# Optimization experiments

Hardware: AMD Instinct MI355X
Metric: run time of the kernel (lower is better)

Reference implementation:

```python
import jax, jax.numpy as jnp
import numpy as np

B, T = 128, 50
VOCAB, EMB_D, GRU_H = 10000, 200, 100
HEADS, AHID, THID = 8, 96, 96

def _conv(x, w, b, pad):
    y = jax.lax.conv_general_dilated(x, w, (1, 1), pad,
        dimension_numbers=('NCHW', 'OIHW', 'NCHW'))
    return y + b[None, :, None, None]

def _bn(x, g, b, m, v):
    s = jax.lax.rsqrt(v + 1e-5)
    return (x - m[None, :, None, None]) * (g * s)[None, :, None, None] + b[None, :, None, None]

def _maxpool(x):
    return jax.lax.reduce_window(x, -jnp.inf, jax.lax.max, (1, 1, 2, 2), (1, 1, 2, 2), 'VALID')

def _resize(x):
    # F.interpolate(mode='bilinear', align_corners=False) == half-pixel bilinear, no antialias
    return jax.image.resize(x, (x.shape[0], x.shape[1], 25, 156), 'bilinear', antialias=False)

def _audio_attn(x, wq, bq, wk, bk, wv, bv):
    # x: [B,96,H,W]; wq: [heads,96,96] == stacked per-head 1x1 convs
    Q = jnp.einsum('bchw,noc->bnohw', x, wq) + bq[None, :, :, None, None]
    K = jnp.einsum('bchw,noc->bnohw', x, wk) + bk[None, :, :, None, None]
    V = jnp.einsum('bchw,noc->bnohw', x, wv) + bv[None, :, :, None, None]
    # torch F.softmax with no dim on a 4D tensor defaults to dim=1 (channels) -> axis=2 here
    return jax.nn.softmax(Q * K, axis=2) * V  # [B,heads,96,H,W]

def _text_attn(o, wq, bq, wk, bk, wv, bv):
    # o: [N,100]; wq: [heads,96,100] == stacked per-head Linear layers
    Q = jnp.einsum('nd,hod->nho', o, wq) + bq[None]
    K = jnp.einsum('nd,hod->nho', o, wk) + bk[None]
    V = jnp.einsum('nd,hod->nho', o, wv) + bv[None]
    a = jax.nn.softmax(Q * K, axis=2) * V  # 2D softmax default dim=1 -> over feature axis
    return a.reshape(o.shape[0], -1)  # head-concat order == torch cat along dim=1

def _gru(xs, w_ih, w_hh, b_ih, b_hh):
    # xs: [T,B,200]; torch gate order r, z, n; b_hn applied inside r-gating
    def step(h, x):
        gi = x @ w_ih.T + b_ih
        gh = h @ w_hh.T + b_hh
        ir, iz, inew = jnp.split(gi, 3, axis=1)
        hr, hz, hnew = jnp.split(gh, 3, axis=1)
        r = jax.nn.sigmoid(ir + hr)
        z = jax.nn.sigmoid(iz + hz)
        n = jnp.tanh(inew + r * hnew)
        h2 = (1.0 - z) * n + z * h
        return h2, h2
    h0 = jnp.zeros((xs.shape[1], GRU_H), xs.dtype)
    hT, outs = jax.lax.scan(step, h0, xs)
    return outs, hT

def _forward(tokens, lengths, mfcc_t, mfcc_f, mfcc_c, w1a, b1a, g1a, be1a, m1a, v1a, w1b, b1b, g1b, be1b, m1b, v1b, w2, b2, g2, be2, m2, v2, w3, b3, g3, be3, m3, v3, w4, b4, g4, be4, m4, v4, wq_a1, bq_a1, wk_a1, bk_a1, wv_a1, bv_a1, wq_a2, bq_a2, wk_a2, bk_a2, wv_a2, bv_a2, emb, w_ih, w_hh, b_ih, b_hh, wq_t1, bq_t1, wk_t1, bk_t1, wv_t1, bv_t1, wq_t2, bq_t2, wk_t2, bk_t2, wv_t2, bv_t2, w_fa, b_fa, w_ft, b_ft, w_e, b_e):
    # --- audio CNN stem (eval-mode batchnorm; dropout off) ---
    xa = jax.nn.relu(_bn(_conv(mfcc_t, w1a, b1a, 'VALID'), g1a, be1a, m1a, v1a))
    xb = jax.nn.relu(_bn(_conv(mfcc_f, w1b, b1b, 'VALID'), g1b, be1b, m1b, v1b))
    # NOTE: original source reuses conv1b/bn1b for the third input (faithful to that)
    xc = jax.nn.relu(_bn(_conv(mfcc_c, w1b, b1b, 'VALID'), g1b, be1b, m1b, v1b))
    x = jnp.concatenate([_resize(xa), _resize(xb), _resize(xc)], axis=1)  # [B,24,25,156]
    x = _maxpool(jax.nn.relu(_bn(_conv(x, w2, b2, [(1, 1), (1, 1)]), g2, be2, m2, v2)))  # [B,32,12,78]
    x = _maxpool(jax.nn.relu(_bn(_conv(x, w3, b3, [(1, 1), (1, 1)]), g3, be3, m3, v3)))  # [B,64,6,39]
    x = jax.nn.relu(_bn(_conv(x, w4, b4, [(1, 1), (1, 1)]), g4, be4, m4, v4))            # [B,96,6,39]
    # --- two stacked per-head audio attentions, then per-head spatial GAP ---
    a1 = _audio_attn(x, wq_a1, bq_a1, wk_a1, bk_a1, wv_a1, bv_a1).mean(axis=(-2, -1))  # [B,8,96]
    a2 = _audio_attn(x, wq_a2, bq_a2, wk_a2, bk_a2, wv_a2, bv_a2).mean(axis=(-2, -1))
    # forward() slices heads along the height concat and GAPs -> per head [stage1 96, stage2 96]
    self_attn_audio = jnp.concatenate([a1, a2], axis=2).reshape(x.shape[0], -1)  # [B,1536]
    # --- text branch: embedding + GRU (all lengths == T -> pack/pad is identity) ---
    ex = jnp.swapaxes(emb[tokens], 0, 1)  # [T,B,200]
    outs, h = _gru(ex, w_ih, w_hh, b_ih, b_hh)  # h: [B,100]
    output = jnp.swapaxes(outs, 0, 1).reshape(-1, GRU_H)  # [B*T,100]
    t1 = _text_attn(output, wq_t1, bq_t1, wk_t1, bk_t1, wv_t1, bv_t1)
    t2 = _text_attn(output, wq_t2, bq_t2, wk_t2, bk_t2, wv_t2, bv_t2)
    self_attn_text = jnp.concatenate([t1, t2], axis=1).reshape(x.shape[0], T, -1).sum(axis=1)  # [B,1536]
    # --- cross-modal gated fusion ---
    x_gap = x.mean(axis=(-2, -1))  # [B,96]
    a_text = jax.nn.softmax(x_gap @ w_fa.T + b_fa, axis=1)   # [B,100]
    attn_text_based_audio = a_text * h                        # [B,100]
    a_audio = jax.nn.softmax(h @ w_ft.T + b_ft, axis=1)      # [B,96]
    attn_audio_based_text = a_audio * x_gap                   # [B,96]
    feat = jnp.concatenate([self_attn_audio, self_attn_text,
                            attn_audio_based_text, attn_text_based_audio], axis=1)  # [B,3268]
    return feat @ w_e.T + b_e  # [B,4] emotion logits

def setup_inputs() -> dict:
    key = jax.random.key(0)
    ks = iter(jax.random.split(key, 100))
    nrm = lambda s, sc=0.05: jax.random.normal(next(ks), s, jnp.float32) * sc
    uni = lambda s: jax.random.uniform(next(ks), s, jnp.float32) * 0.5 + 0.5
    d = {}
    d['mfcc_t'] = jax.random.normal(next(ks), (B, 1, 200, 40), jnp.float32)
    d['mfcc_f'] = jax.random.normal(next(ks), (B, 1, 200, 40), jnp.float32)
    d['mfcc_c'] = jax.random.normal(next(ks), (B, 1, 200, 40), jnp.float32)
    d['tokens'] = jax.random.randint(next(ks), (B, T), 0, VOCAB)
    d['lengths'] = jnp.full((B,), T, jnp.int32)
    def bnp(pre, c):
        d['g' + pre] = 1.0 + nrm((c,)); d['be' + pre] = nrm((c,))
        d['m' + pre] = nrm((c,)); d['v' + pre] = uni((c,))
    d['w1a'] = nrm((8, 1, 5, 2), 0.2); d['b1a'] = nrm((8,)); bnp('1a', 8)
    d['w1b'] = nrm((8, 1, 2, 6), 0.2); d['b1b'] = nrm((8,)); bnp('1b', 8)
    d['w2'] = nrm((32, 24, 3, 3), 0.1); d['b2'] = nrm((32,)); bnp('2', 32)
    d['w3'] = nrm((64, 32, 3, 3), 0.1); d['b3'] = nrm((64,)); bnp('3', 64)
    d['w4'] = nrm((96, 64, 3, 3), 0.08); d['b4'] = nrm((96,)); bnp('4', 96)
    for s in ('1', '2'):
        for p in ('q', 'k', 'v'):
            d['w%s_a%s' % (p, s)] = nrm((HEADS, 96, 96), 0.1)
            d['b%s_a%s' % (p, s)] = nrm((HEADS, 96))
    d['emb'] = nrm((VOCAB, EMB_D), 0.1)
    d['w_ih'] = nrm((3 * GRU_H, EMB_D), 0.1); d['w_hh'] = nrm((3 * GRU_H, GRU_H), 0.1)
    d['b_ih'] = nrm((3 * GRU_H,)); d['b_hh'] = nrm((3 * GRU_H,))
    for s in ('1', '2'):
        for p in ('q', 'k', 'v'):
            d['w%s_t%s' % (p, s)] = nrm((HEADS, THID, GRU_H), 0.1)
            d['b%s_t%s' % (p, s)] = nrm((HEADS, THID))
    d['w_fa'] = nrm((100, 96), 0.1); d['b_fa'] = nrm((100,))
    d['w_ft'] = nrm((96, 100), 0.1); d['b_ft'] = nrm((96,))
    d['w_e'] = nrm((4, 2 * HEADS * AHID + 2 * HEADS * THID + 96 + 100), 0.05); d['b_e'] = nrm((4,))
    return d

def reference(mfcc_t, mfcc_f, mfcc_c, tokens, lengths, w1a, b1a, g1a, be1a, m1a, v1a, w1b, b1b, g1b, be1b, m1b, v1b, w2, b2, g2, be2, m2, v2, w3, b3, g3, be3, m3, v3, w4, b4, g4, be4, m4, v4, wq_a1, bq_a1, wk_a1, bk_a1, wv_a1, bv_a1, wq_a2, bq_a2, wk_a2, bk_a2, wv_a2, bv_a2, emb, w_ih, w_hh, b_ih, b_hh, wq_t1, bq_t1, wk_t1, bk_t1, wv_t1, bv_t1, wq_t2, bq_t2, wk_t2, bk_t2, wv_t2, bv_t2, w_fa, b_fa, w_ft, b_ft, w_e, b_e):
    return _forward(tokens, lengths, mfcc_t, mfcc_f, mfcc_c, w1a, b1a, g1a, be1a, m1a, v1a, w1b, b1b, g1b, be1b, m1b, v1b, w2, b2, g2, be2, m2, v2, w3, b3, g3, be3, m3, v3, w4, b4, g4, be4, m4, v4, wq_a1, bq_a1, wk_a1, bk_a1, wv_a1, bv_a1, wq_a2, bq_a2, wk_a2, bk_a2, wv_a2, bv_a2, emb, w_ih, w_hh, b_ih, b_hh, wq_t1, bq_t1, wk_t1, bk_t1, wv_t1, bv_t1, wq_t2, bq_t2, wk_t2, bk_t2, wv_t2, bv_t2, w_fa, b_fa, w_ft, b_ft, w_e, b_e)
```

## Files before the change

kernel.cpp:

```cpp
#include <hip/hip_runtime.h>
#include <math.h>

static constexpr int kB = 128;
static constexpr int kT = 50;

struct TDesc { const float* src; float* dst; int O; int C; int total; };
struct TPack { TDesc d[15]; };
__global__ void k_transpose_pack(TPack p) {
    TDesc t = p.d[blockIdx.y];
    int idx = blockIdx.x * 256 + threadIdx.x;
    if (idx >= t.total) return;
    int o = idx % t.O; int r = idx / t.O; int c = r % t.C; int n = r / t.C;
    t.dst[idx] = t.src[((size_t)n * t.O + o) * t.C + c];
}

__global__ void k_stem(const float* __restrict__ mt, const float* __restrict__ mf,
                       const float* __restrict__ mc,
                       const float* __restrict__ w1a, const float* __restrict__ b1a,
                       const float* __restrict__ g1a, const float* __restrict__ be1a,
                       const float* __restrict__ m1a, const float* __restrict__ v1a,
                       const float* __restrict__ w1b, const float* __restrict__ b1b,
                       const float* __restrict__ g1b, const float* __restrict__ be1b,
                       const float* __restrict__ m1b, const float* __restrict__ v1b,
                       float* __restrict__ out, int total) {
    int idx = blockIdx.x * blockDim.x + threadIdx.x;
    if (idx >= total) return;
    int ox = idx % 156; int t = idx / 156;
    int oy = t % 25; t /= 25;
    int ch = t % 24; int b = t / 24;
    int grp = ch >> 3, c = ch & 7;
    const float* src; int Hc, Wc;
    const float *wb, *cb, *g, *be, *m, *v;
    if (grp == 0) { src = mt; Hc = 196; Wc = 39; wb = w1a + c * 10;
                    cb = b1a; g = g1a; be = be1a; m = m1a; v = v1a; }
    else          { src = (grp == 1 ? mf : mc); Hc = 199; Wc = 35; wb = w1b + c * 12;
                    cb = b1b; g = g1b; be = be1b; m = m1b; v = v1b; }
    float s = g[c] * rsqrtf(v[c] + 1e-5f);
    float bias = (cb[c] - m[c]) * s + be[c];
    float sy = (oy + 0.5f) * ((float)Hc / 25.f) - 0.5f;
    float sx = (ox + 0.5f) * ((float)Wc / 156.f) - 0.5f;
    float fy0 = floorf(sy), fx0 = floorf(sx);
    float fy = sy - fy0, fx = sx - fx0;
    int y0 = (int)fy0, x0 = (int)fx0;
    int y0c = min(max(y0, 0), Hc - 1), y1c = min(max(y0 + 1, 0), Hc - 1);
    int x0c = min(max(x0, 0), Wc - 1), x1c = min(max(x0 + 1, 0), Wc - 1);
    bool xs = (x1c == x0c), ys = (y1c == y0c);
    const float* p = src + (size_t)b * 8000;
    float t00, t01, t10, t11;
    if (grp == 0) {
        float W[6][3];
        #pragma unroll
        for (int r = 0; r < 6; ++r) {
            int rr = min(y0c + r, 199);
            #pragma unroll
            for (int cc = 0; cc < 3; ++cc)
                W[r][cc] = p[rr * 40 + min(x0c + cc, 39)];
        }
        float a00 = 0.f, a01 = 0.f, a10 = 0.f, a11 = 0.f;
        #pragma unroll
        for (int ky = 0; ky < 5; ++ky)
            #pragma unroll
            for (int kx = 0; kx < 2; ++kx) {
                float wv = wb[ky * 2 + kx];
                a00 += W[ky][kx] * wv;     a01 += W[ky][kx + 1] * wv;
                a10 += W[ky + 1][kx] * wv; a11 += W[ky + 1][kx + 1] * wv;
            }
        t00 = a00;
        t01 = xs ? a00 : a01;
        t10 = ys ? a00 : a10;
        t11 = xs ? (ys ? a00 : a10) : (ys ? a01 : a11);
    } else {
        float W[3][7];
        #pragma unroll
        for (int r = 0; r < 3; ++r) {
            int rr = min(y0c + r, 199);
            #pragma unroll
            for (int cc = 0; cc < 7; ++cc)
                W[r][cc] = p[rr * 40 + min(x0c + cc, 39)];
        }
        float a00 = 0.f, a01 = 0.f, a10 = 0.f, a11 = 0.f;
        #pragma unroll
        for (int ky = 0; ky < 2; ++ky)
            #pragma unroll
            for (int kx = 0; kx < 6; ++kx) {
                float wv = wb[ky * 6 + kx];
                a00 += W[ky][kx] * wv;     a01 += W[ky][kx + 1] * wv;
                a10 += W[ky + 1][kx] * wv; a11 += W[ky + 1][kx + 1] * wv;
            }
        t00 = a00;
        t01 = xs ? a00 : a01;
        t10 = ys ? a00 : a10;
        t11 = xs ? (ys ? a00 : a10) : (ys ? a01 : a11);
    }
    float r00 = fmaxf(t00 * s + bias, 0.f), r01 = fmaxf(t01 * s + bias, 0.f);
    float r10 = fmaxf(t10 * s + bias, 0.f), r11 = fmaxf(t11 * s + bias, 0.f);
    out[idx] = r00 * (1.f - fy) * (1.f - fx) + r01 * (1.f - fy) * fx
// ... 20 lines not shown
    for (int j = 0; j < NPX; ++j) {
        int px = tid + j * 256;
        int oy = px / W, ox = px - oy * W;
        bool ok = (px < ROWS * W) && (row0 + oy < H);
        val[j] = ok;
        off[j] = ok ? (oy * WP + ox) : 0;
    }

    float acc[NPX][8];
    #pragma unroll
    for (int j = 0; j < NPX; ++j)
        #pragma unroll
        for (int o = 0; o < 8; ++o) acc[j][o] = 0.f;

    for (int c0 = 0; c0 < CIN; c0 += CI_T) {
        __syncthreads();
        for (int e = tid; e < STAGE; e += 256) {
            int ci = e / (RP * WP);
            int rem = e - ci * RP * WP;
            int r = rem / WP;
            int xx = rem - r * WP;
            int iy = row0 - 1 + r;
            int ix = xx - 1;
            float vv = 0.f;
            if (iy >= 0 && iy < H && ix >= 0 && ix < W)
                vv = in[((size_t)(b * CIN + c0 + ci) * H + iy) * W + ix];
            sx[e] = vv;
        }
        for (int e = tid; e < CI_T * 9 * 8; e += 256) {
            int rk = e >> 3;
            int o = e & 7;
            sw[e] = wT[((size_t)c0 * 9 + rk) * COUT + oc0 + o];
        }
        __syncthreads();
        #pragma unroll 1
        for (int cl = 0; cl < CI_T; ++cl) {
            const float* sxc = sx + cl * RP * WP;
            #pragma unroll
            for (int k = 0; k < 9; ++k) {
                const int ky = k / 3, kx = k % 3;
                const float4 wa = *(const float4*)(sw + (cl * 9 + k) * 8);
                const float4 wb = *(const float4*)(sw + (cl * 9 + k) * 8 + 4);
                #pragma unroll
                for (int j = 0; j < NPX; ++j) {
                    float xv = sxc[off[j] + ky * WP + kx];
                    acc[j][0] += xv * wa.x; acc[j][1] += xv * wa.y;
                    acc[j][2] += xv * wa.z; acc[j][3] += xv * wa.w;
                    acc[j][4] += xv * wb.x; acc[j][5] += xv * wb.y;
                    acc[j][6] += xv * wb.z; acc[j][7] += xv * wb.w;
                }
            }
        }
    }
    float sc[8], bi[8];
    #pragma unroll
    for (int o = 0; o < 8; ++o) {
        float s = g[oc0 + o] * rsqrtf(v[oc0 + o] + 1e-5f);
        sc[o] = s; bi[o] = (cb[oc0 + o] - m[oc0 + o]) * s + be[oc0 + o];
    }
    #pragma unroll
    for (int j = 0; j < NPX; ++j) if (val[j]) {
        int px = tid + j * 256;
        int oy = row0 + px / W, ox = px % W;
        #pragma unroll
        for (int o = 0; o < 8; ++o)
            out[((size_t)(b * COUT + oc0 + o) * H + oy) * W + ox] =
                fmaxf(acc[j][o] * sc[o] + bi[o], 0.f);
    }
}

__global__ void k_maxpool(const float* __restrict__ in, float* __restrict__ out,
                          int C, int Hin, int Win, int Hout, int Wout, int total) {
    int idx = blockIdx.x * blockDim.x + threadIdx.x;
    if (idx >= total) return;
    int ox = idx % Wout; int t = idx / Wout;
    int oy = t % Hout; t /= Hout;
    int c = t % C; int b = t / C;
    const float* p = in + ((size_t)(b * C + c) * Hin + 2 * oy) * Win + 2 * ox;
    float m0 = fmaxf(p[0], p[1]);
    float m1 = fmaxf(p[Win], p[Win + 1]);
    out[idx] = fmaxf(m0, m1);
}

__global__ void __launch_bounds__(128) k_audio_attn(
    const float* __restrict__ x,
    const float* __restrict__ wq1, const float* __restrict__ bq1,
    const float* __restrict__ wk1, const float* __restrict__ bk1,
    const float* __restrict__ wv1, const float* __restrict__ bv1,
    const float* __restrict__ wq2, const float* __restrict__ bq2,
    const float* __restrict__ wk2, const float* __restrict__ bk2,
    const float* __restrict__ wv2, const float* __restrict__ bv2,
    float* __restrict__ afeat, float* __restrict__ xgap) {
    int b = blockIdx.x, n = blockIdx.y, stage = blockIdx.z;
    const float* wq = stage ? wq2 : wq1; const float* bq = stage ? bq2 : bq1;
    const float* wk = stage ? wk2 : wk1; const float* bk = stage ? bk2 : bk1;
    const float* wv = stage ? wv2 : wv1; const float* bv = stage ? bv2 : bv1;
    __shared__ float xt[96 * 28];
    __shared__ float sb[96 * 27];
    __shared__ float pmax[4][26], psum[4][26];
    __shared__ float mx[26], sm[26];
    int tid = threadIdx.x;
    bool act = tid < 96;
    int o = act ? tid : 0;
    float bqv = act ? bq[n * 96 + tid] : 0.f;
    float bkv = act ? bk[n * 96 + tid] : 0.f;
    float bvv = act ? bv[n * 96 + tid] : 0.f;
    const float* wqb = wq + n * 9216 + o;
    const float* wkb = wk + n * 9216 + o;
    const float* wvb = wv + n * 9216 + o;
    const bool do_gap = (n == 0 && stage == 0);
    float accO = 0.f, xsum = 0.f;
    const float* xb = x + (size_t)b * 96 * 234;
    for (int tile = 0; tile < 9; ++tile) {
        int p0 = tile * 26;
        __syncthreads();
        for (int e = tid; e < 2496; e += 128) {
            int c = e / 26, pp = e - c * 26;
            xt[c * 28 + pp] = xb[c * 234 + p0 + pp];
        }
        __syncthreads();
        if (do_gap && act) {
            const float* xr = xt + o * 28;
            #pragma unroll
            for (int p = 0; p < 26; ++p) xsum += xr[p];
        }
        float aq[26], ak[26], av[26];
        #pragma unroll
        for (int p = 0; p < 26; ++p) { aq[p] = bqv; ak[p] = bkv; av[p] = bvv; }
        for (int c = 0; c < 96; ++c) {
            float wqv = wqb[c * 96], wkv = wkb[c * 96], wvv2 = wvb[c * 96];
            const float* xr = xt + c * 28;
            #pragma unroll
            for (int q4 = 0; q4 < 6; ++q4) {
                float4 x4 = *(const float4*)(xr + q4 * 4);
                int p = q4 * 4;
                aq[p]   += wqv * x4.x; ak[p]   += wkv * x4.x; av[p]   += wvv2 * x4.x;
                aq[p+1] += wqv * x4.y; ak[p+1] += wkv * x4.y; av[p+1] += wvv2 * x4.y;
                aq[p+2] += wqv * x4.z; ak[p+2] += wkv * x4.z; av[p+2] += wvv2 * x4.z;
                aq[p+3] += wqv * x4.w; ak[p+3] += wkv * x4.w; av[p+3] += wvv2 * x4.w;
            }
            float2 x2 = *(const float2*)(xr + 24);
            aq[24] += wqv * x2.x; ak[24] += wkv * x2.x; av[24] += wvv2 * x2.x;
            aq[25] += wqv * x2.y; ak[25] += wkv * x2.y; av[25] += wvv2 * x2.y;
        }
        if (act) {
            #pragma unroll
            for (int p = 0; p < 26; ++p)
                sb[o * 27 + p] = aq[p] * ak[p];
        }
        __syncthreads();
        if (tid < 104) {
            int p = tid % 26, ch = tid / 26;
            int o0 = ch * 24;
            float m_ = -1e30f;
            for (int q = 0; q < 24; ++q) m_ = fmaxf(m_, sb[(o0 + q) * 27 + p]);
            pmax[ch][p] = m_;
        }
        __syncthreads();
        if (tid < 26)
            mx[tid] = fmaxf(fmaxf(pmax[0][tid], pmax[1][tid]),
                            fmaxf(pmax[2][tid], pmax[3][tid]));
        __syncthreads();
        if (tid < 104) {
            int p = tid % 26, ch = tid / 26;
            int o0 = ch * 24;
            float mv = mx[p];
            float s_ = 0.f;
            for (int q = 0; q < 24; ++q) s_ += __expf(sb[(o0 + q) * 27 + p] - mv);
            psum[ch][p] = s_;
        }
        __syncthreads();
        if (tid < 26)
            sm[tid] = psum[0][tid] + psum[1][tid] + psum[2][tid] + psum[3][tid];
        __syncthreads();
        if (act) {
            #pragma unroll
            for (int p = 0; p < 26; ++p)
                accO += __expf(sb[o * 27 + p] - mx[p]) / sm[p] * av[p];
        }
    }
    if (act) afeat[b * 1536 + n * 192 + stage * 96 + tid] = accO * (1.f / 234.f);
    if (do_gap && act) xgap[b * 96 + tid] = xsum * (1.f / 234.f);
}

__global__ void __launch_bounds__(320) k_gi(const int* __restrict__ tokens,
        const float* __restrict__ emb, const float* __restrict__ w_ih,
        const float* __restrict__ b_ih, float* __restrict__ GI) {
    int r0 = blockIdx.x * 8;
    int tid = threadIdx.x;
    __shared__ float er[8][200];
    for (int e = tid; e < 1600; e += 320) {
        int r = e / 200, c = e - r * 200;
        er[r][c] = emb[(size_t)tokens[r0 + r] * 200 + c];
    }
    __syncthreads();
    if (tid < 300) {
        float acc[8];
        float bv = b_ih[tid];
        #pragma unroll
        for (int r = 0; r < 8; ++r) acc[r] = bv;
        for (int k4 = 0; k4 < 50; ++k4) {
            float4 w4 = *(const float4*)(w_ih + (size_t)tid * 200 + k4 * 4);
            #pragma unroll
            for (int r = 0; r < 8; ++r) {
                float4 x4 = *(const float4*)&er[r][k4 * 4];
                acc[r] += w4.x * x4.x + w4.y * x4.y + w4.z * x4.z + w4.w * x4.w;
            }
        }
        #pragma unroll
        for (int r = 0; r < 8; ++r)
            GI[(size_t)(r0 + r) * 300 + tid] = acc[r];
    }
}

__global__ void __launch_bounds__(320) k_gru_all(const float* __restrict__ GI,
        const float* __restrict__ w_hh, const float* __restrict__ b_hh,
        float* __restrict__ outs) {
    int b = blockIdx.x, tid = threadIdx.x;
    __shared__ float hs[100];
    __shared__ float gH[300];
    float4 wreg[25];
    float bias = 0.f;
    if (tid < 300) {
        bias = b_hh[tid];
        #pragma unroll
        for (int k4 = 0; k4 < 25; ++k4)
            wreg[k4] = *(const float4*)(w_hh + (size_t)tid * 100 + k4 * 4);
    }
    if (tid < 100) hs[tid] = 0.f;
    __syncthreads();
    for (int t = 0; t < kT; ++t) {
        if (tid < 300) {
            float gh = bias;
            #pragma unroll
            for (int k4 = 0; k4 < 25; ++k4) {
                float4 h4 = *(const float4*)&hs[k4 * 4];
                gh += wreg[k4].x * h4.x + wreg[k4].y * h4.y
                    + wreg[k4].z * h4.z + wreg[k4].w * h4.w;
            }
            gH[tid] = gh;
        }
        __syncthreads();
        if (tid < 100) {
            const float* gi = GI + ((size_t)b * kT + t) * 300;
            float r = 1.f / (1.f + expf(-(gi[tid] + gH[tid])));
            float z = 1.f / (1.f + expf(-(gi[100 + tid] + gH[100 + tid])));
            float nn = tanhf(gi[200 + tid] + r * gH[200 + tid]);
            float h2 = (1.f - z) * nn + z * hs[tid];
            hs[tid] = h2;
            outs[((size_t)b * kT + t) * 100 + tid] = h2;
        }
        __syncthreads();
    }
}

__global__ void __launch_bounds__(128) k_text_attn(const float* __restrict__ outs,
    const float* __restrict__ wq1, const float* __restrict__ bq1,
    const float* __restrict__ wk1, const float* __restrict__ bk1,
    const float* __restrict__ wv1, const float* __restrict__ bv1,
    const float* __restrict__ wq2, const float* __restrict__ bq2,
    const float* __restrict__ wk2, const float* __restrict__ bk2,
    const float* __restrict__ wv2, const float* __restrict__ bv2,
    float* __restrict__ tfeat) {
    int b = blockIdx.x, stage = blockIdx.y, n = blockIdx.z;
    const float* wq = stage ? wq2 : wq1; const float* bq = stage ? bq2 : bq1;
// ... 107 lines not shown
    }
    __syncthreads();
    if (tid < 100) atba[tid] = expf(st[tid] - redm[0]) / reds[0] * hv[tid];
    if (tid < 96)  aat[tid]  = expf(sa[tid] - redm[1]) / reds[1] * xg[tid];
    __syncthreads();
    float a0 = 0.f, a1 = 0.f, a2 = 0.f, a3 = 0.f;
    for (int col = tid; col < 3268; col += 128) {
        float f;
        if (col < 1536)      f = afeat[b * 1536 + col];
        else if (col < 3072) f = tfeat[b * 1536 + col - 1536];
        else if (col < 3168) f = aat[col - 3072];
        else                 f = atba[col - 3168];
        a0 += w_e[col] * f;            a1 += w_e[3268 + col] * f;
        a2 += w_e[2 * 3268 + col] * f; a3 += w_e[3 * 3268 + col] * f;
    }
    __shared__ float r4[4][128];
    r4[0][tid] = a0; r4[1][tid] = a1; r4[2][tid] = a2; r4[3][tid] = a3;
    __syncthreads();
    if (tid < 4) {
        float s = 0.f;
        for (int i = 0; i < 128; ++i) s += r4[tid][i];
        out[b * 4 + tid] = s + b_e[tid];
    }
}

extern "C" void kernel_launch(void* const* d_in, const int* in_sizes, int n_in,
                              void* d_out, int out_size, void* d_ws, size_t ws_size,
                              hipStream_t stream) {
    (void)in_sizes; (void)n_in; (void)out_size; (void)ws_size;
    const float* mfcc_t = (const float*)d_in[0];
    const float* mfcc_f = (const float*)d_in[1];
    const float* mfcc_c = (const float*)d_in[2];
    const int*   tokens = (const int*)d_in[3];
    const float *w1a = (const float*)d_in[5],  *b1a = (const float*)d_in[6],
                *g1a = (const float*)d_in[7],  *be1a = (const float*)d_in[8],
                *m1a = (const float*)d_in[9],  *v1a = (const float*)d_in[10];
    const float *w1b = (const float*)d_in[11], *b1b = (const float*)d_in[12],
                *g1b = (const float*)d_in[13], *be1b = (const float*)d_in[14],
                *m1b = (const float*)d_in[15], *v1b = (const float*)d_in[16];
    const float *w2 = (const float*)d_in[17], *b2 = (const float*)d_in[18],
                *g2 = (const float*)d_in[19], *be2 = (const float*)d_in[20],
                *m2 = (const float*)d_in[21], *v2 = (const float*)d_in[22];
    const float *w3 = (const float*)d_in[23], *b3 = (const float*)d_in[24],
                *g3 = (const float*)d_in[25], *be3 = (const float*)d_in[26],
                *m3 = (const float*)d_in[27], *v3 = (const float*)d_in[28];
    const float *w4 = (const float*)d_in[29], *b4 = (const float*)d_in[30],
                *g4 = (const float*)d_in[31], *be4 = (const float*)d_in[32],
                *m4 = (const float*)d_in[33], *v4 = (const float*)d_in[34];
    const float *wq_a1 = (const float*)d_in[35], *bq_a1 = (const float*)d_in[36],
                *wk_a1 = (const float*)d_in[37], *bk_a1 = (const float*)d_in[38],
                *wv_a1 = (const float*)d_in[39], *bv_a1 = (const float*)d_in[40];
    const float *wq_a2 = (const float*)d_in[41], *bq_a2 = (const float*)d_in[42],
                *wk_a2 = (const float*)d_in[43], *bk_a2 = (const float*)d_in[44],
                *wv_a2 = (const float*)d_in[45], *bv_a2 = (const float*)d_in[46];
    const float *emb  = (const float*)d_in[47];
    const float *w_ih = (const float*)d_in[48], *w_hh = (const float*)d_in[49],
                *b_ih = (const float*)d_in[50], *b_hh = (const float*)d_in[51];
    const float *wq_t1 = (const float*)d_in[52], *bq_t1 = (const float*)d_in[53],
                *wk_t1 = (const float*)d_in[54], *bk_t1 = (const float*)d_in[55],
                *wv_t1 = (const float*)d_in[56], *bv_t1 = (const float*)d_in[57];
    const float *wq_t2 = (const float*)d_in[58], *bq_t2 = (const float*)d_in[59],
                *wk_t2 = (const float*)d_in[60], *bk_t2 = (const float*)d_in[61],
                *wv_t2 = (const float*)d_in[62], *bv_t2 = (const float*)d_in[63];
    const float *w_fa = (const float*)d_in[64], *b_fa = (const float*)d_in[65],
                *w_ft = (const float*)d_in[66], *b_ft = (const float*)d_in[67],
                *w_e  = (const float*)d_in[68], *b_e  = (const float*)d_in[69];

    float* ws = (float*)d_ws;
    const size_t Z0 = 0;
    const size_t Z1 = 22091776ull;
    const size_t OUTS  = 34072576ull;
    const size_t AFEAT = 34712576ull;
    const size_t TFEAT = 34909184ull;
    const size_t XGAP  = 35105792ull;
    const size_t WT    = 35118080ull;
    float* X1 = ws + Z1;
    float* C2 = ws + Z0;  float* P2 = ws + Z1;
    float* C3 = ws + Z0;  float* P3 = ws + Z1;
    float* X4 = ws + Z0;  float* GI = ws + Z1;
    float* outs  = ws + OUTS;
    float* afeat = ws + AFEAT;
    float* tfeat = ws + TFEAT;
    float* xgap  = ws + XGAP;
    float* wqa1t = ws + WT;
    float* wka1t = wqa1t + 73728; float* wva1t = wka1t + 73728;
    float* wqa2t = wva1t + 73728; float* wka2t = wqa2t + 73728; float* wva2t = wka2t + 73728;
    float* wqt1t = wva2t + 73728;
    float* wkt1t = wqt1t + 76800; float* wvt1t = wkt1t + 76800;
    float* wqt2t = wvt1t + 76800; float* wkt2t = wqt2t + 76800; float* wvt2t = wkt2t + 76800;
    float* wT2 = outs;
    float* wT3 = outs + 6912;
    float* wT4 = outs + 25344;

    TPack tp;
    tp.d[0]  = {wq_a1, wqa1t, 96, 96, 73728};
    tp.d[1]  = {wk_a1, wka1t, 96, 96, 73728};
    tp.d[2]  = {wv_a1, wva1t, 96, 96, 73728};
    tp.d[3]  = {wq_a2, wqa2t, 96, 96, 73728};
    tp.d[4]  = {wk_a2, wka2t, 96, 96, 73728};
    tp.d[5]  = {wv_a2, wva2t, 96, 96, 73728};
    tp.d[6]  = {w2, wT2, 32, 216, 6912};
    tp.d[7]  = {w3, wT3, 64, 288, 18432};
    tp.d[8]  = {w4, wT4, 96, 576, 55296};
    tp.d[9]  = {wq_t1, wqt1t, 96, 100, 76800};
    tp.d[10] = {wk_t1, wkt1t, 96, 100, 76800};
    tp.d[11] = {wv_t1, wvt1t, 96, 100, 76800};
    tp.d[12] = {wq_t2, wqt2t, 96, 100, 76800};
    tp.d[13] = {wk_t2, wkt2t, 96, 100, 76800};
    tp.d[14] = {wv_t2, wvt2t, 96, 100, 76800};
    k_transpose_pack<<<dim3(300, 15), 256, 0, stream>>>(tp);

    k_stem<<<46800, 256, 0, stream>>>(mfcc_t, mfcc_f, mfcc_c,
        w1a, b1a, g1a, be1a, m1a, v1a,
        w1b, b1b, g1b, be1b, m1b, v1b, X1, 11980800);
    k_conv3x3_tiled<24, 8, 25, 156, 9, 6><<<dim3(128, 3, 4), 256, 0, stream>>>(
        X1, wT2, b2, g2, be2, m2, v2, C2, 32);
    k_maxpool<<<14976, 256, 0, stream>>>(C2, P2, 32, 25, 156, 12, 78, 3833856);
    k_conv3x3_tiled<32, 8, 12, 78, 12, 4><<<dim3(128, 1, 8), 256, 0, stream>>>(
        P2, wT3, b3, g3, be3, m3, v3, C3, 64);
    k_maxpool<<<7488, 256, 0, stream>>>(C3, P3, 64, 12, 78, 6, 39, 1916928);
    k_conv3x3_tiled<64, 16, 6, 39, 6, 1><<<dim3(128, 1, 12), 256, 0, stream>>>(
        P3, wT4, b4, g4, be4, m4, v4, X4, 96);

    k_audio_attn<<<dim3(kB, 8, 2), 128, 0, stream>>>(X4,
        wqa1t, bq_a1, wka1t, bk_a1, wva1t, bv_a1,
        wqa2t, bq_a2, wka2t, bk_a2, wva2t, bv_a2, afeat, xgap);

    k_gi<<<kB * kT / 8, 320, 0, stream>>>(tokens, emb, w_ih, b_ih, GI);
    k_gru_all<<<kB, 320, 0, stream>>>(GI, w_hh, b_hh, outs);
    k_text_attn<<<dim3(kB, 2, 8), 128, 0, stream>>>(outs,
        wqt1t, bq_t1, wkt1t, bk_t1, wvt1t, bv_t1,
        wqt2t, bq_t2, wkt2t, bk_t2, wvt2t, bv_t2, tfeat);

    k_final<<<kB, 128, 0, stream>>>(xgap, outs, afeat, tfeat,
                                    w_fa, b_fa, w_ft, b_ft, w_e, b_e, (float*)d_out);
}
```

Before: 1.571 ms.

## Restructure audio attention kernel to parallelize over positions with atomic reductions

The audio attention kernel now splits each batch item's 234 spatial positions across 4 blocks of 256 threads. Each thread holds one position's 96 channels in registers and reads untransposed weight rows staged through shared memory with a register prefetch. The softmax over channels is computed in a single pass, and the per-channel mean over positions is reduced with wave shuffles plus atomicAdd into a buffer zeroed beforehand. This exposes more parallelism and drops the per-tile syncs and the audio weight transposes, in exchange for a large register footprint, atomics, and an extra zeroing launch.

```diff
diff --git a/kernel.cpp b/kernel.cpp
--- a/kernel.cpp
+++ b/kernel.cpp
@@ -5,13 +5,19 @@
 static constexpr int kT = 50;
 
 struct TDesc { const float* src; float* dst; int O; int C; int total; };
-struct TPack { TDesc d[15]; };
+struct TPack { TDesc d[9]; };
 __global__ void k_transpose_pack(TPack p) {
     TDesc t = p.d[blockIdx.y];
     int idx = blockIdx.x * 256 + threadIdx.x;
     if (idx >= t.total) return;
     int o = idx % t.O; int r = idx / t.O; int c = r % t.C; int n = r / t.C;
     t.dst[idx] = t.src[((size_t)n * t.O + o) * t.C + c];
+}
+
+__global__ void k_zero2(float* __restrict__ a, int na, float* __restrict__ b, int nb) {
+    int i = blockIdx.x * 256 + threadIdx.x;
+    if (i < na) a[i] = 0.f;
+    if (i < nb) b[i] = 0.f;
 }
 
 __global__ void k_stem(const float* __restrict__ mt, const float* __restrict__ mf,
@@ -198,7 +204,7 @@
     out[idx] = fmaxf(m0, m1);
 }
 
-__global__ void __launch_bounds__(128) k_audio_attn(
+__global__ void __launch_bounds__(256, 2) k_audio_attn(
     const float* __restrict__ x,
     const float* __restrict__ wq1, const float* __restrict__ bq1,
     const float* __restrict__ wk1, const float* __restrict__ bk1,
@@ -207,96 +213,165 @@
     const float* __restrict__ wk2, const float* __restrict__ bk2,
     const float* __restrict__ wv2, const float* __restrict__ bv2,
     float* __restrict__ afeat, float* __restrict__ xgap) {
-    int b = blockIdx.x, n = blockIdx.y, stage = blockIdx.z;
+    const int b = blockIdx.x >> 2, pt = blockIdx.x & 3;
+    const int n = blockIdx.y, stage = blockIdx.z;
     const float* wq = stage ? wq2 : wq1; const float* bq = stage ? bq2 : bq1;
     const float* wk = stage ? wk2 : wk1; const float* bk = stage ? bk2 : bk1;
     const float* wv = stage ? wv2 : wv1; const float* bv = stage ? bv2 : bv1;
-    __shared__ float xt[96 * 28];
-    __shared__ float sb[96 * 27];
-    __shared__ float pmax[4][26], psum[4][26];
-    __shared__ float mx[26], sm[26];
-    int tid = threadIdx.x;
-    bool act = tid < 96;
-    int o = act ? tid : 0;
-    float bqv = act ? bq[n * 96 + tid] : 0.f;
-    float bkv = act ? bk[n * 96 + tid] : 0.f;
-    float bvv = act ? bv[n * 96 + tid] : 0.f;
-    const float* wqb = wq + n * 9216 + o;
-    const float* wkb = wk + n * 9216 + o;
-    const float* wvb = wv + n * 9216 + o;
-    const bool do_gap = (n == 0 && stage == 0);
-    float accO = 0.f, xsum = 0.f;
-    const float* xb = x + (size_t)b * 96 * 234;
-    for (int tile = 0; tile < 9; ++tile) {
-        int p0 = tile * 26;
-        __syncthreads();
-        for (int e = tid; e < 2496; e += 128) {
-            int c = e / 26, pp = e - c * 26;
-            xt[c * 28 + pp] = xb[c * 234 + p0 + pp];
-        }
-        __syncthreads();
-        if (do_gap && act) {
-            const float* xr = xt + o * 28;
-            #pragma unroll
-            for (int p = 0; p < 26; ++p) xsum += xr[p];
-        }
-        float aq[26], ak[26], av[26];
-        #pragma unroll
-        for (int p = 0; p < 26; ++p) { aq[p] = bqv; ak[p] = bkv; av[p] = bvv; }
+    const int tid = threadIdx.x;
+    const int p = tid & 63, og = tid >> 6;
+    const int gp = pt * 64 + p;
+    const bool pact = gp < 234;
+
+    __shared__ float sS[96][64];
+    __shared__ float swb[3072];
+    __shared__ float pm[4][64];
+    __shared__ float zz[4][64];
+
+    float xr[96];
+    const float* xb = x + (size_t)b * (96 * 234) + gp;
+    #pragma unroll
+    for (int c = 0; c < 96; ++c) {
+        float vld = 0.f;
+        if (pact) vld = xb[c * 234];
+        xr[c] = vld;
+    }
+
+    if (n == 0 && stage == 0 && og == 0) {
+        #pragma unroll
         for (int c = 0; c < 96; ++c) {
-            float wqv = wqb[c * 96], wkv = wkb[c * 96], wvv2 = wvb[c * 96];
-            const float* xr = xt + c * 28;
-            #pragma unroll
-            for (int q4 = 0; q4 < 6; ++q4) {
-                float4 x4 = *(const float4*)(xr + q4 * 4);
-                int p = q4 * 4;
-                aq[p]   += wqv * x4.x; ak[p]   += wkv * x4.x; av[p]   += wvv2 * x4.x;
-                aq[p+1] += wqv * x4.y; ak[p+1] += wkv * x4.y; av[p+1] += wvv2 * x4.y;
-                aq[p+2] += wqv * x4.z; ak[p+2] += wkv * x4.z; av[p+2] += wvv2 * x4.z;
-                aq[p+3] += wqv * x4.w; ak[p+3] += wkv * x4.w; av[p+3] += wvv2 * x4.w;
-            }
-            float2 x2 = *(const float2*)(xr + 24);
-            aq[24] += wqv * x2.x; ak[24] += wkv * x2.x; av[24] += wvv2 * x2.x;
-            aq[25] += wqv * x2.y; ak[25] += wkv * x2.y; av[25] += wvv2 * x2.y;
-        }
-        if (act) {
-            #pragma unroll
-            for (int p = 0; p < 26; ++p)
-                sb[o * 27 + p] = aq[p] * ak[p];
-        }
-        __syncthreads();
-        if (tid < 104) {
-            int p = tid % 26, ch = tid / 26;
-            int o0 = ch * 24;
-            float m_ = -1e30f;
-            for (int q = 0; q < 24; ++q) m_ = fmaxf(m_, sb[(o0 + q) * 27 + p]);
-            pmax[ch][p] = m_;
-        }
-        __syncthreads();
-        if (tid < 26)
-            mx[tid] = fmaxf(fmaxf(pmax[0][tid], pmax[1][tid]),
-                            fmaxf(pmax[2][tid], pmax[3][tid]));
-        __syncthreads();
-        if (tid < 104) {
-            int p = tid % 26, ch = tid / 26;
-            int o0 = ch * 24;
-            float mv = mx[p];
-            float s_ = 0.f;
-            for (int q = 0; q < 24; ++q) s_ += __expf(sb[(o0 + q) * 27 + p] - mv);
-            psum[ch][p] = s_;
-        }
-        __syncthreads();
-        if (tid < 26)
-            sm[tid] = psum[0][tid] + psum[1][tid] + psum[2][tid] + psum[3][tid];
-        __syncthreads();
-        if (act) {
-            #pragma unroll
-            for (int p = 0; p < 26; ++p)
-                accO += __expf(sb[o * 27 + p] - mx[p]) / sm[p] * av[p];
-        }
-    }
-    if (act) afeat[b * 1536 + n * 192 + stage * 96 + tid] = accO * (1.f / 234.f);
-    if (do_gap && act) xgap[b * 96 + tid] = xsum * (1.f / 234.f);
+            float v = xr[c];
+            #pragma unroll
+            for (int off = 1; off < 64; off <<= 1) v += __shfl_xor(v, off);
+            if (p == 0) atomicAdd(&xgap[b * 96 + c], v * (1.f / 234.f));
+        }
+    }
+
+    const float* wqn = wq + n * 9216;
+    const float* wkn = wk + n * 9216;
+    const float* wvn = wv + n * 9216;
+    const float* bqn = bq + n * 96;
+    const float* bkn = bk + n * 96;
+    const float* bvn = bv + n * 96;
+
+    float pmax = -1e30f;
+
+    {
+        float rb[12];
+        #pragma unroll
+        for (int j = 0; j < 6; ++j) rb[j] = wqn[j * 256 + tid];
+        #pragma unroll
+        for (int j = 0; j < 6; ++j) rb[6 + j] = wkn[j * 256 + tid];
+        #pragma unroll
+        for (int j = 0; j < 6; ++j) swb[j * 256 + tid] = rb[j];
+        #pragma unroll
+        for (int j = 0; j < 6; ++j) swb[1536 + j * 256 + tid] = rb[6 + j];
+        for (int oc = 0; oc < 6; ++oc) {
+            float rn[12];
+            if (oc < 5) {
+                const float* qp = wqn + (oc + 1) * 1536;
+                const float* kp = wkn + (oc + 1) * 1536;
+                #pragma unroll
+                for (int j = 0; j < 6; ++j) rn[j] = qp[j * 256 + tid];
+                #pragma unroll
+                for (int j = 0; j < 6; ++j) rn[6 + j] = kp[j * 256 + tid];
+            }
+            __syncthreads();
+            #pragma unroll
+            for (int oi = 0; oi < 4; ++oi) {
+                const int ol = oi * 4 + og;
+                const int o = oc * 16 + ol;
+                const float* wqr = swb + ol * 96;
+                const float* wkr = swb + 1536 + ol * 96;
+                float qa = bqn[o], qb = 0.f, ka = bkn[o], kb = 0.f;
+                #pragma unroll
+                for (int c8 = 0; c8 < 12; ++c8) {
+                    float4 w0 = *(const float4*)(wqr + c8 * 8);
+                    float4 w1 = *(const float4*)(wqr + c8 * 8 + 4);
+                    float4 u0 = *(const float4*)(wkr + c8 * 8);
+                    float4 u1 = *(const float4*)(wkr + c8 * 8 + 4);
+                    qa += w0.x * xr[c8 * 8 + 0] + w0.y * xr[c8 * 8 + 1]
+                        + w0.z * xr[c8 * 8 + 2] + w0.w * xr[c8 * 8 + 3];
+                    qb += w1.x * xr[c8 * 8 + 4] + w1.y * xr[c8 * 8 + 5]
+                        + w1.z * xr[c8 * 8 + 6] + w1.w * xr[c8 * 8 + 7];
+                    ka += u0.x * xr[c8 * 8 + 0] + u0.y * xr[c8 * 8 + 1]
+                        + u0.z * xr[c8 * 8 + 2] + u0.w * xr[c8 * 8 + 3];
+                    kb += u1.x * xr[c8 * 8 + 4] + u1.y * xr[c8 * 8 + 5]
+                        + u1.z * xr[c8 * 8 + 6] + u1.w * xr[c8 * 8 + 7];
+                }
+                float s = (qa + qb) * (ka + kb);
+                sS[o][p] = s;
+                pmax = fmaxf(pmax, s);
+            }
+            __syncthreads();
+            if (oc < 5) {
+                #pragma unroll
+                for (int j = 0; j < 6; ++j) swb[j * 256 + tid] = rn[j];
+                #pragma unroll
+                for (int j = 0; j < 6; ++j) swb[1536 + j * 256 + tid] = rn[6 + j];
+            }
+        }
+    }
+
+    pm[og][p] = pmax;
+    __syncthreads();
+    const float m = fmaxf(fmaxf(pm[0][p], pm[1][p]), fmaxf(pm[2][p], pm[3][p]));
+    float zp = 0.f;
+    #pragma unroll
+    for (int k = 0; k < 24; ++k) {
+        const int o = (k >> 2) * 16 + (k & 3) * 4 + og;
+        float e = __expf(sS[o][p] - m);
+        sS[o][p] = e;
+        zp += e;
+    }
+    zz[og][p] = zp;
+    __syncthreads();
+    const float rZ = 1.f / (zz[0][p] + zz[1][p] + zz[2][p] + zz[3][p]);
+    const float scale = pact ? rZ * (1.f / 234.f) : 0.f;
+
+    {
+        float rv[6];
+        #pragma unroll
+        for (int j = 0; j < 6; ++j) rv[j] = wvn[j * 256 + tid];
+        #pragma unroll
+        for (int j = 0; j < 6; ++j) swb[j * 256 + tid] = rv[j];
+        float* aout = afeat + b * 1536 + n * 192 + stage * 96;
+        for (int oc = 0; oc < 6; ++oc) {
+            float rn[6];
+            if (oc < 5) {
+                const float* vp = wvn + (oc + 1) * 1536;
+                #pragma unroll
+                for (int j = 0; j < 6; ++j) rn[j] = vp[j * 256 + tid];
+            }
+            __syncthreads();
+            #pragma unroll
+            for (int oi = 0; oi < 4; ++oi) {
+                const int ol = oi * 4 + og;
+                const int o = oc * 16 + ol;
+                const float* wvr = swb + ol * 96;
+                float va = bvn[o], vb = 0.f;
+                #pragma unroll
+                for (int c8 = 0; c8 < 12; ++c8) {
+                    float4 w0 = *(const float4*)(wvr + c8 * 8);
+                    float4 w1 = *(const float4*)(wvr + c8 * 8 + 4);
+                    va += w0.x * xr[c8 * 8 + 0] + w0.y * xr[c8 * 8 + 1]
+                        + w0.z * xr[c8 * 8 + 2] + w0.w * xr[c8 * 8 + 3];
+                    vb += w1.x * xr[c8 * 8 + 4] + w1.y * xr[c8 * 8 + 5]
+                        + w1.z * xr[c8 * 8 + 6] + w1.w * xr[c8 * 8 + 7];
+                }
+                float contrib = sS[o][p] * scale * (va + vb);
+                #pragma unroll
+                for (int off = 1; off < 64; off <<= 1)
+                    contrib += __shfl_xor(contrib, off);
+                if (p == 0) atomicAdd(aout + o, contrib);
+            }
+            __syncthreads();
+            if (oc < 5) {
+                #pragma unroll
+                for (int j = 0; j < 6; ++j) swb[j * 256 + tid] = rn[j];
+            }
+        }
+    }
 }
 
 __global__ void __launch_bounds__(320) k_gi(const int* __restrict__ tokens,
@@ -570,10 +645,7 @@
     float* afeat = ws + AFEAT;
     float* tfeat = ws + TFEAT;
     float* xgap  = ws + XGAP;
-    float* wqa1t = ws + WT;
-    float* wka1t = wqa1t + 73728; float* wva1t = wka1t + 73728;
-    float* wqa2t = wva1t + 73728; float* wka2t = wqa2t + 73728; float* wva2t = wka2t + 73728;
-    float* wqt1t = wva2t + 73728;
+    float* wqt1t = ws + WT;
     float* wkt1t = wqt1t + 76800; float* wvt1t = wkt1t + 76800;
     float* wqt2t = wvt1t + 76800; float* wkt2t = wqt2t + 76800; float* wvt2t = wkt2t + 76800;
     float* wT2 = outs;
@@ -581,22 +653,18 @@
     float* wT4 = outs + 25344;
 
     TPack tp;
-    tp.d[0]  = {wq_a1, wqa1t, 96, 96, 73728};
-    tp.d[1]  = {wk_a1, wka1t, 96, 96, 73728};
-    tp.d[2]  = {wv_a1, wva1t, 96, 96, 73728};
-    tp.d[3]  = {wq_a2, wqa2t, 96, 96, 73728};
-    tp.d[4]  = {wk_a2, wka2t, 96, 96, 73728};
-    tp.d[5]  = {wv_a2, wva2t, 96, 96, 73728};
-    tp.d[6]  = {w2, wT2, 32, 216, 6912};
-    tp.d[7]  = {w3, wT3, 64, 288, 18432};
-    tp.d[8]  = {w4, wT4, 96, 576, 55296};
-    tp.d[9]  = {wq_t1, wqt1t, 96, 100, 76800};
-    tp.d[10] = {wk_t1, wkt1t, 96, 100, 76800};
-    tp.d[11] = {wv_t1, wvt1t, 96, 100, 76800};
-    tp.d[12] = {wq_t2, wqt2t, 96, 100, 76800};
-    tp.d[13] = {wk_t2, wkt2t, 96, 100, 76800};
-    tp.d[14] = {wv_t2, wvt2t, 96, 100, 76800};
-    k_transpose_pack<<<dim3(300, 15), 256, 0, stream>>>(tp);
+    tp.d[0] = {w2, wT2, 32, 216, 6912};
+    tp.d[1] = {w3, wT3, 64, 288, 18432};
+    tp.d[2] = {w4, wT4, 96, 576, 55296};
+    tp.d[3] = {wq_t1, wqt1t, 96, 100, 76800};
+    tp.d[4] = {wk_t1, wkt1t, 96, 100, 76800};
+    tp.d[5] = {wv_t1, wvt1t, 96, 100, 76800};
+    tp.d[6] = {wq_t2, wqt2t, 96, 100, 76800};
+    tp.d[7] = {wk_t2, wkt2t, 96, 100, 76800};
+    tp.d[8] = {wv_t2, wvt2t, 96, 100, 76800};
+    k_transpose_pack<<<dim3(300, 9), 256, 0, stream>>>(tp);
+
+    k_zero2<<<768, 256, 0, stream>>>(afeat, 196608, xgap, 12288);
 
     k_stem<<<46800, 256, 0, stream>>>(mfcc_t, mfcc_f, mfcc_c,
         w1a, b1a, g1a, be1a, m1a, v1a,
@@ -610,9 +678,9 @@
     k_conv3x3_tiled<64, 16, 6, 39, 6, 1><<<dim3(128, 1, 12), 256, 0, stream>>>(
         P3, wT4, b4, g4, be4, m4, v4, X4, 96);
 
-    k_audio_attn<<<dim3(kB, 8, 2), 128, 0, stream>>>(X4,
-        wqa1t, bq_a1, wka1t, bk_a1, wva1t, bv_a1,
-        wqa2t, bq_a2, wka2t, bk_a2, wva2t, bv_a2, afeat, xgap);
+    k_audio_attn<<<dim3(kB * 4, 8, 2), 256, 0, stream>>>(X4,
+        wq_a1, bq_a1, wk_a1, bk_a1, wv_a1, bv_a1,
+        wq_a2, bq_a2, wk_a2, bk_a2, wv_a2, bv_a2, afeat, xgap);
 
     k_gi<<<kB * kT / 8, 320, 0, stream>>>(tokens, emb, w_ih, b_ih, GI);
     k_gru_all<<<kB, 320, 0, stream>>>(GI, w_hh, b_hh, outs);
```

Result: slower. 1.823 ms (+16.1%).

## Retile audio attention into register-blocked GEMM with position splits and atomics

Applied to the files above, without the earlier changes.

The audio attention kernel is rewritten so that each block handles a 64-position slice of one sample, head and stage, with 256 threads. Each thread register-blocks 6 output channels by 4 positions, and weights are staged through shared memory in 8-channel chunks. Partial position sums are combined with atomicAdd, which needs a zeroing kernel beforehand. The global-average-pool reduction moves into its own kernel. The goal is higher occupancy and better data reuse than the old design, where 96 threads each kept 78 accumulators and read weights straight from global memory. In exchange it adds a zeroing launch, floating-point atomics and padded positions in the last slice.

```diff
diff --git a/kernel.cpp b/kernel.cpp
--- a/kernel.cpp
+++ b/kernel.cpp
@@ -12,6 +12,11 @@
     if (idx >= t.total) return;
     int o = idx % t.O; int r = idx / t.O; int c = r % t.C; int n = r / t.C;
     t.dst[idx] = t.src[((size_t)n * t.O + o) * t.C + c];
+}
+
+__global__ void k_zero(float* __restrict__ a, int n) {
+    int i = blockIdx.x * 256 + threadIdx.x;
+    if (i < n) a[i] = 0.f;
 }
 
 __global__ void k_stem(const float* __restrict__ mt, const float* __restrict__ mf,
@@ -198,7 +203,21 @@
     out[idx] = fmaxf(m0, m1);
 }
 
-__global__ void __launch_bounds__(128) k_audio_attn(
+__global__ void __launch_bounds__(256) k_xgap(const float* __restrict__ x,
+                                              float* __restrict__ xgap) {
+    int b = blockIdx.x, tid = threadIdx.x;
+    int wave = tid >> 6, lane = tid & 63;
+    for (int c = wave; c < 96; c += 4) {
+        const float* row = x + ((size_t)b * 96 + c) * 234;
+        float s = 0.f;
+        for (int p = lane; p < 234; p += 64) s += row[p];
+        #pragma unroll
+        for (int off = 1; off < 64; off <<= 1) s += __shfl_xor(s, off);
+        if (lane == 0) xgap[b * 96 + c] = s * (1.f / 234.f);
+    }
+}
+
+__global__ void __launch_bounds__(256, 4) k_audio_attn(
     const float* __restrict__ x,
     const float* __restrict__ wq1, const float* __restrict__ bq1,
     const float* __restrict__ wk1, const float* __restrict__ bk1,
@@ -206,97 +225,139 @@
     const float* __restrict__ wq2, const float* __restrict__ bq2,
     const float* __restrict__ wk2, const float* __restrict__ bk2,
     const float* __restrict__ wv2, const float* __restrict__ bv2,
-    float* __restrict__ afeat, float* __restrict__ xgap) {
-    int b = blockIdx.x, n = blockIdx.y, stage = blockIdx.z;
-    const float* wq = stage ? wq2 : wq1; const float* bq = stage ? bq2 : bq1;
-    const float* wk = stage ? wk2 : wk1; const float* bk = stage ? bk2 : bk1;
-    const float* wv = stage ? wv2 : wv1; const float* bv = stage ? bv2 : bv1;
-    __shared__ float xt[96 * 28];
-    __shared__ float sb[96 * 27];
-    __shared__ float pmax[4][26], psum[4][26];
-    __shared__ float mx[26], sm[26];
-    int tid = threadIdx.x;
-    bool act = tid < 96;
-    int o = act ? tid : 0;
-    float bqv = act ? bq[n * 96 + tid] : 0.f;
-    float bkv = act ? bk[n * 96 + tid] : 0.f;
-    float bvv = act ? bv[n * 96 + tid] : 0.f;
-    const float* wqb = wq + n * 9216 + o;
-    const float* wkb = wk + n * 9216 + o;
-    const float* wvb = wv + n * 9216 + o;
-    const bool do_gap = (n == 0 && stage == 0);
-    float accO = 0.f, xsum = 0.f;
-    const float* xb = x + (size_t)b * 96 * 234;
-    for (int tile = 0; tile < 9; ++tile) {
-        int p0 = tile * 26;
-        __syncthreads();
-        for (int e = tid; e < 2496; e += 128) {
-            int c = e / 26, pp = e - c * 26;
-            xt[c * 28 + pp] = xb[c * 234 + p0 + pp];
-        }
-        __syncthreads();
-        if (do_gap && act) {
-            const float* xr = xt + o * 28;
-            #pragma unroll
-            for (int p = 0; p < 26; ++p) xsum += xr[p];
-        }
-        float aq[26], ak[26], av[26];
-        #pragma unroll
-        for (int p = 0; p < 26; ++p) { aq[p] = bqv; ak[p] = bkv; av[p] = bvv; }
-        for (int c = 0; c < 96; ++c) {
-            float wqv = wqb[c * 96], wkv = wkb[c * 96], wvv2 = wvb[c * 96];
-            const float* xr = xt + c * 28;
-            #pragma unroll
-            for (int q4 = 0; q4 < 6; ++q4) {
-                float4 x4 = *(const float4*)(xr + q4 * 4);
-                int p = q4 * 4;
-                aq[p]   += wqv * x4.x; ak[p]   += wkv * x4.x; av[p]   += wvv2 * x4.x;
-                aq[p+1] += wqv * x4.y; ak[p+1] += wkv * x4.y; av[p+1] += wvv2 * x4.y;
-                aq[p+2] += wqv * x4.z; ak[p+2] += wkv * x4.z; av[p+2] += wvv2 * x4.z;
-                aq[p+3] += wqv * x4.w; ak[p+3] += wkv * x4.w; av[p+3] += wvv2 * x4.w;
-            }
-            float2 x2 = *(const float2*)(xr + 24);
-            aq[24] += wqv * x2.x; ak[24] += wkv * x2.x; av[24] += wvv2 * x2.x;
-            aq[25] += wqv * x2.y; ak[25] += wkv * x2.y; av[25] += wvv2 * x2.y;
-        }
-        if (act) {
-            #pragma unroll
-            for (int p = 0; p < 26; ++p)
-                sb[o * 27 + p] = aq[p] * ak[p];
-        }
-        __syncthreads();
-        if (tid < 104) {
-            int p = tid % 26, ch = tid / 26;
-            int o0 = ch * 24;
-            float m_ = -1e30f;
-            for (int q = 0; q < 24; ++q) m_ = fmaxf(m_, sb[(o0 + q) * 27 + p]);
-            pmax[ch][p] = m_;
-        }
-        __syncthreads();
-        if (tid < 26)
-            mx[tid] = fmaxf(fmaxf(pmax[0][tid], pmax[1][tid]),
-                            fmaxf(pmax[2][tid], pmax[3][tid]));
-        __syncthreads();
-        if (tid < 104) {
-            int p = tid % 26, ch = tid / 26;
-            int o0 = ch * 24;
-            float mv = mx[p];
-            float s_ = 0.f;
-            for (int q = 0; q < 24; ++q) s_ += __expf(sb[(o0 + q) * 27 + p] - mv);
-            psum[ch][p] = s_;
-        }
-        __syncthreads();
-        if (tid < 26)
-            sm[tid] = psum[0][tid] + psum[1][tid] + psum[2][tid] + psum[3][tid];
-        __syncthreads();
-        if (act) {
-            #pragma unroll
-            for (int p = 0; p < 26; ++p)
-                accO += __expf(sb[o * 27 + p] - mx[p]) / sm[p] * av[p];
-        }
-    }
-    if (act) afeat[b * 1536 + n * 192 + stage * 96 + tid] = accO * (1.f / 234.f);
-    if (do_gap && act) xgap[b * 96 + tid] = xsum * (1.f / 234.f);
+    float* __restrict__ afeat) {
+    const int b = blockIdx.x >> 2, pt = blockIdx.x & 3;
+    const int n = blockIdx.y, stage = blockIdx.z;
+    const float* wq = (stage ? wq2 : wq1) + n * 9216;
+    const float* wk = (stage ? wk2 : wk1) + n * 9216;
+    const float* wv = (stage ? wv2 : wv1) + n * 9216;
+    const float* bqn = (stage ? bq2 : bq1) + n * 96;
+    const float* bkn = (stage ? bk2 : bk1) + n * 96;
+    const float* bvn = (stage ? bv2 : bv1) + n * 96;
+    const int tid = threadIdx.x;
+    const int to = tid >> 4, tp = tid & 15;
+    const int ob = to * 6;
+    const int p0 = pt * 64;
+
+    __shared__ float sx[96 * 64];
+    __shared__ float sw[2304];
+    __shared__ float sred[1536];
+
+    {
+        const float* xb = x + (size_t)b * (96 * 234) + p0;
+        for (int e = tid; e < 96 * 64; e += 256) {
+            int c = e >> 6, p = e & 63;
+            sx[e] = (p0 + p < 234) ? xb[c * 234 + p] : 0.f;
+        }
+    }
+
+    float qa[6][4], ka[6][4], va[6][4];
+    #pragma unroll
+    for (int j = 0; j < 6; ++j)
+        #pragma unroll
+        for (int i = 0; i < 4; ++i) { qa[j][i] = 0.f; ka[j][i] = 0.f; va[j][i] = 0.f; }
+
+    for (int c0 = 0; c0 < 96; c0 += 8) {
+        __syncthreads();
+        {
+            const int base = c0 * 96;
+            for (int e4 = tid; e4 < 576; e4 += 256) {
+                int mat = (e4 >= 384) ? 2 : (e4 >= 192 ? 1 : 0);
+                int r4 = e4 - mat * 192;
+                const float* wsrc = (mat == 0) ? wq : (mat == 1 ? wk : wv);
+                *(float4*)(sw + e4 * 4) = *(const float4*)(wsrc + base + r4 * 4);
+            }
+        }
+        __syncthreads();
+        #pragma unroll 2
+        for (int cc = 0; cc < 8; ++cc) {
+            float4 x4 = *(const float4*)(sx + (c0 + cc) * 64 + tp * 4);
+            const float* wr = sw + cc * 96 + ob;
+            float2 q01 = *(const float2*)(wr);
+            float2 q23 = *(const float2*)(wr + 2);
+            float2 q45 = *(const float2*)(wr + 4);
+            float2 k01 = *(const float2*)(wr + 768);
+            float2 k23 = *(const float2*)(wr + 770);
+            float2 k45 = *(const float2*)(wr + 772);
+            float2 v01 = *(const float2*)(wr + 1536);
+            float2 v23 = *(const float2*)(wr + 1538);
+            float2 v45 = *(const float2*)(wr + 1540);
+            float wqv[6] = {q01.x, q01.y, q23.x, q23.y, q45.x, q45.y};
+            float wkv[6] = {k01.x, k01.y, k23.x, k23.y, k45.x, k45.y};
+            float wvv[6] = {v01.x, v01.y, v23.x, v23.y, v45.x, v45.y};
+            #pragma unroll
+            for (int j = 0; j < 6; ++j) {
+                qa[j][0] += wqv[j] * x4.x; qa[j][1] += wqv[j] * x4.y;
+                qa[j][2] += wqv[j] * x4.z; qa[j][3] += wqv[j] * x4.w;
+                ka[j][0] += wkv[j] * x4.x; ka[j][1] += wkv[j] * x4.y;
+                ka[j][2] += wkv[j] * x4.z; ka[j][3] += wkv[j] * x4.w;
+                va[j][0] += wvv[j] * x4.x; va[j][1] += wvv[j] * x4.y;
+                va[j][2] += wvv[j] * x4.z; va[j][3] += wvv[j] * x4.w;
+            }
+        }
+    }
+
+    float bqv[6], bkv[6], bvv[6];
+    #pragma unroll
+    for (int j = 0; j < 6; ++j) {
+        bqv[j] = bqn[ob + j]; bkv[j] = bkn[ob + j]; bvv[j] = bvn[ob + j];
+    }
+    float pmx[4] = {-1e30f, -1e30f, -1e30f, -1e30f};
+    #pragma unroll
+    for (int j = 0; j < 6; ++j)
+        #pragma unroll
+        for (int i = 0; i < 4; ++i) {
+            float sv = (qa[j][i] + bqv[j]) * (ka[j][i] + bkv[j]);
+            qa[j][i] = sv;
+            pmx[i] = fmaxf(pmx[i], sv);
+        }
+    __syncthreads();
+    #pragma unroll
+    for (int i = 0; i < 4; ++i) sred[to * 64 + tp * 4 + i] = pmx[i];
+    __syncthreads();
+    float m_[4];
+    #pragma unroll
+    for (int i = 0; i < 4; ++i) {
+        float mm = -1e30f;
+        for (int t = 0; t < 16; ++t) mm = fmaxf(mm, sred[t * 64 + tp * 4 + i]);
+        m_[i] = mm;
+    }
+    __syncthreads();
+    float z[4] = {0.f, 0.f, 0.f, 0.f};
+    #pragma unroll
+    for (int j = 0; j < 6; ++j)
+        #pragma unroll
+        for (int i = 0; i < 4; ++i) {
+            float e = __expf(qa[j][i] - m_[i]);
+            qa[j][i] = e;
+            z[i] += e;
+        }
+    #pragma unroll
+    for (int i = 0; i < 4; ++i) sred[to * 64 + tp * 4 + i] = z[i];
+    __syncthreads();
+    float rz[4];
+    #pragma unroll
+    for (int i = 0; i < 4; ++i) {
+        float zs = 0.f;
+        for (int t = 0; t < 16; ++t) zs += sred[t * 64 + tp * 4 + i];
+        rz[i] = (p0 + tp * 4 + i < 234) ? 1.f / zs : 0.f;
+    }
+    __syncthreads();
+    #pragma unroll
+    for (int j = 0; j < 6; ++j) {
+        float po = qa[j][0] * rz[0] * (va[j][0] + bvv[j])
+                 + qa[j][1] * rz[1] * (va[j][1] + bvv[j])
+                 + qa[j][2] * rz[2] * (va[j][2] + bvv[j])
+                 + qa[j][3] * rz[3] * (va[j][3] + bvv[j]);
+        sred[(ob + j) * 16 + tp] = po;
+    }
+    __syncthreads();
+    if (tid < 96) {
+        float ssum = 0.f;
+        #pragma unroll
+        for (int t = 0; t < 16; ++t) ssum += sred[tid * 16 + t];
+        atomicAdd(afeat + b * 1536 + n * 192 + stage * 96 + tid, ssum * (1.f / 234.f));
+    }
 }
 
 __global__ void __launch_bounds__(320) k_gi(const int* __restrict__ tokens,
@@ -598,6 +659,8 @@
     tp.d[14] = {wv_t2, wvt2t, 96, 100, 76800};
     k_transpose_pack<<<dim3(300, 15), 256, 0, stream>>>(tp);
 
+    k_zero<<<768, 256, 0, stream>>>(afeat, 196608);
+
     k_stem<<<46800, 256, 0, stream>>>(mfcc_t, mfcc_f, mfcc_c,
         w1a, b1a, g1a, be1a, m1a, v1a,
         w1b, b1b, g1b, be1b, m1b, v1b, X1, 11980800);
@@ -610,9 +673,11 @@
     k_conv3x3_tiled<64, 16, 6, 39, 6, 1><<<dim3(128, 1, 12), 256, 0, stream>>>(
         P3, wT4, b4, g4, be4, m4, v4, X4, 96);
 
-    k_audio_attn<<<dim3(kB, 8, 2), 128, 0, stream>>>(X4,
+    k_xgap<<<kB, 256, 0, stream>>>(X4, xgap);
+
+    k_audio_attn<<<dim3(kB * 4, 8, 2), 256, 0, stream>>>(X4,
         wqa1t, bq_a1, wka1t, bk_a1, wva1t, bv_a1,
-        wqa2t, bq_a2, wka2t, bk_a2, wva2t, bv_a2, afeat, xgap);
+        wqa2t, bq_a2, wka2t, bk_a2, wva2t, bv_a2, afeat);
 
     k_gi<<<kB * kT / 8, 320, 0, stream>>>(tokens, emb, w_ih, b_ih, GI);
     k_gru_all<<<kB, 320, 0, stream>>>(GI, w_hh, b_hh, outs);
```

Result: faster. 1.462 ms (-6.9%).
